# Kernel optimization log

Measured on AMD Instinct MI355X. Metric: run time of the kernel, lower is better.

## Reference

```python
import jax, jax.numpy as jnp
import numpy as np

N_NODES = 50000
N_EDGES = 800000
DIM_IN = 128
DIM_H = 128
DIM_OUT = 10
N_GRAPHS = 256


def _glorot(key, shape):
    lim = float(np.sqrt(6.0 / (shape[0] + shape[1])))
    return jax.random.uniform(key, shape, jnp.float32, -lim, lim)


def setup_inputs() -> dict:
    key = jax.random.key(0)
    ks = jax.random.split(key, 8)
    x = jax.random.normal(ks[0], (N_NODES, DIM_IN), jnp.float32)
    edge_index = jax.random.randint(ks[1], (2, N_EDGES), 0, N_NODES, dtype=jnp.int64)
    batch = jnp.sort(jax.random.randint(ks[2], (N_NODES,), 0, N_GRAPHS, dtype=jnp.int64))
    return {
        'x': x,
        'edge_index': edge_index,
        'batch': batch,
        'W1': _glorot(ks[3], (DIM_IN, DIM_H)),
        'b1': jnp.zeros((DIM_H,), jnp.float32),
        'W2': _glorot(ks[4], (DIM_H, DIM_H)),
        'b2': jnp.zeros((DIM_H,), jnp.float32),
        'Wl1': _glorot(ks[5], (2 * DIM_H, 2 * DIM_H)),
        'bl1': jnp.zeros((2 * DIM_H,), jnp.float32),
        'Wl2': _glorot(ks[6], (2 * DIM_H, DIM_OUT)),
        'bl2': jnp.zeros((DIM_OUT,), jnp.float32),
    }


def _gcn_conv(h, W, b, src, dst, norm, n):
    # x @ W, gather source rows, scale by symmetric norm, scatter-add to dest
    m = (h @ W)[src] * norm[:, None]          # [E+N, dim_h]
    return jax.ops.segment_sum(m, dst, num_segments=n) + b


def reference(x, edge_index, batch, W1, b1, W2, b2, Wl1, bl1, Wl2, bl2):
    n = x.shape[0]
    loops = jnp.arange(n, dtype=edge_index.dtype)
    src = jnp.concatenate([edge_index[0], loops])  # add self-loops (PyG GCNConv default)
    dst = jnp.concatenate([edge_index[1], loops])
    deg = jax.ops.segment_sum(jnp.ones_like(dst, x.dtype), dst, num_segments=n)
    dinv = jnp.where(deg > 0, jax.lax.rsqrt(jnp.maximum(deg, 1.0)), 0.0)
    norm = dinv[src] * dinv[dst]
    # eval mode: dropout is identity
    h1 = _gcn_conv(x, W1, b1, src, dst, norm, n)
    h2 = _gcn_conv(h1, W2, b2, src, dst, norm, n)
    g1 = jax.ops.segment_sum(h1, batch, num_segments=N_GRAPHS)  # global_add_pool
    g2 = jax.ops.segment_sum(h2, batch, num_segments=N_GRAPHS)
    g = jnp.concatenate([g1, g2], axis=1)  # [N_GRAPHS, 2*dim_h]
    h = jax.nn.relu(g @ Wl1 + bl1)
    h = h @ Wl2 + bl2
    return (h, jax.nn.log_softmax(h, axis=1))
```

## Files before the change

kernel.cpp:

```cpp
#include <hip/hip_runtime.h>
#include <hip/hip_bf16.h>
#include <math.h>


#define DIMH 128
#define EBCAP 8192

typedef __attribute__((ext_vector_type(8))) short s16x8;
typedef __attribute__((ext_vector_type(4))) float f32x4;

__device__ inline ushort f2b(float f) {
    uint u = __float_as_uint(f);
    return (ushort)((u + 0x7fffu + ((u >> 16) & 1u)) >> 16);
}
__device__ inline uint pack2(float lo, float hi) {
    return (uint)f2b(lo) | ((uint)f2b(hi) << 16);
}
__device__ inline float blo(uint u) { return __uint_as_float(u << 16); }
__device__ inline float bhi(uint u) { return __uint_as_float(u & 0xffff0000u); }


#define SCAT_CHUNK 8192
__global__ __launch_bounds__(256) void k_scatter(const int* __restrict__ src,
                                                 const int* __restrict__ dst,
                                                 int* __restrict__ bcnt,
                                                 uint* __restrict__ ebuf, int E) {
    __shared__ int hist[256];
    __shared__ int base[256];
    hist[threadIdx.x] = 0;
    __syncthreads();
    int e0 = blockIdx.x * SCAT_CHUNK;
    int e1 = e0 + SCAT_CHUNK; if (e1 > E) e1 = E;
    for (int e = e0 + threadIdx.x; e < e1; e += 256)
        atomicAdd(&hist[dst[e] >> 8], 1);
    __syncthreads();
    {
        int i = threadIdx.x;
        int h = hist[i];
        base[i] = h ? atomicAdd(&bcnt[i], h) : 0;
        hist[i] = 0;
    }
    __syncthreads();
    for (int e = e0 + threadIdx.x; e < e1; e += 256) {
        int d = dst[e];
        int bk = d >> 8;
        int rank = base[bk] + atomicAdd(&hist[bk], 1);
        if (rank < EBCAP)
            ebuf[(size_t)bk * EBCAP + rank] = ((uint)(d & 255) << 24) | (uint)src[e];
    }
}

__global__ __launch_bounds__(256) void k_bcsr(const uint* __restrict__ ebuf,
                                              const int* __restrict__ bcnt,
                                              float* __restrict__ dinv,
                                              int2* __restrict__ rng,
                                              int* __restrict__ srt, int n) {
    __shared__ int cnt[256];
    __shared__ int wsum[4];
    __shared__ int stage[EBCAP];
    int b = blockIdx.x;
    int t = threadIdx.x;
    int c = bcnt[b]; if (c > EBCAP) c = EBCAP;
    size_t B = (size_t)b * EBCAP;
    cnt[t] = 0;
    __syncthreads();
    for (int i = t; i < c; i += 256)
        atomicAdd(&cnt[ebuf[B + i] >> 24], 1);
    __syncthreads();
    int v = cnt[t];
    int incl = v;
    for (int k = 1; k < 64; k <<= 1) {
        int u = __shfl_up(incl, k, 64);
        if ((t & 63) >= k) incl += u;
    }
    if ((t & 63) == 63) wsum[t >> 6] = incl;
    __syncthreads();
    int add = 0;
    for (int j = 0; j < (t >> 6); ++j) add += wsum[j];
    incl += add;
    int loc = incl - v;
    int node = b * 256 + t;
    if (node < n) {
        dinv[node] = rsqrtf((float)(v + 1));
        rng[node] = make_int2((int)B + loc, (int)B + loc + v);
    }
    cnt[t] = loc;
    __syncthreads();
    for (int i = t; i < c; i += 256) {
        uint r = ebuf[B + i];
        int p = atomicAdd(&cnt[r >> 24], 1);
        stage[p] = (int)(r & 0xffffffu);
    }
    __syncthreads();
    for (int i = t; i < c; i += 256) srt[B + i] = stage[i];
}

__global__ __launch_bounds__(256) void k_wprep(const float* __restrict__ W1,
                                               const float* __restrict__ W2,
                                               ushort* __restrict__ WT1,
                                               ushort* __restrict__ WT2) {
    int idx = blockIdx.x * 256 + threadIdx.x;
    const float* W = (idx < 16384) ? W1 : W2;
    ushort* WT = (idx < 16384) ? WT1 : WT2;
    int t = idx & 16383;
    int k = t >> 7, nn = t & 127;
    WT[nn * 128 + k] = f2b(W[t]);
}

template<bool F32IN>
__global__ __launch_bounds__(256) void k_gemm_mfma(const void* __restrict__ Xin,
                                                   const ushort* __restrict__ WT,
                                                   const float* __restrict__ scale,
                                                   ushort* __restrict__ P, int n) {
    __shared__ ushort lds[64 * 128 + 128 * 128];
    ushort* Xs = lds;
    ushort* Ws = lds + 64 * 128;
    const int tid = threadIdx.x;
    const int row0 = blockIdx.x * 64;
    if (F32IN) {
        const float* Xf = (const float*)Xin;
        for (int ci = tid; ci < 2048; ci += 256) {
            int r = ci >> 5, c8 = ci & 31;
            uint dstB = (uint)(r * 256 + c8 * 8) ^ (uint)((r & 7) << 4);
            uint2 v = make_uint2(0u, 0u);
            if (row0 + r < n) {
                float4 f = *(const float4*)(Xf + (size_t)(row0 + r) * 128 + c8 * 4);
                v.x = pack2(f.x, f.y); v.y = pack2(f.z, f.w);
            }
            *(uint2*)((char*)Xs + dstB) = v;
        }
    } else {
        const ushort* Xb = (const ushort*)Xin;
        for (int ci = tid; ci < 1024; ci += 256) {
            int r = ci >> 4, c16 = ci & 15;
            uint dstB = (uint)(r * 256 + c16 * 16) ^ (uint)((r & 7) << 4);
            uint4 v = make_uint4(0u, 0u, 0u, 0u);
            if (row0 + r < n) v = *(const uint4*)(Xb + (size_t)(row0 + r) * 128 + c16 * 8);
            *(uint4*)((char*)Xs + dstB) = v;
        }
    }
    for (int ci = tid; ci < 2048; ci += 256) {
        int r = ci >> 4, c16 = ci & 15;
        uint dstB = (uint)(r * 256 + c16 * 16) ^ (uint)((r & 7) << 4);
        *(uint4*)((char*)Ws + dstB) = *(const uint4*)(WT + (size_t)r * 128 + c16 * 8);
    }
    __syncthreads();
    const int wave = tid >> 6, lane = tid & 63;
    const int l15 = lane & 15, g = lane >> 4;
    f32x4 acc[8];
#pragma unroll
    for (int nt = 0; nt < 8; ++nt) acc[nt] = (f32x4){0.f, 0.f, 0.f, 0.f};
    const int tr = wave * 16 + l15;
    const uint aswz = (uint)((tr & 7) << 4);
#pragma unroll
    for (int kk = 0; kk < 4; ++kk) {
        uint aB = ((uint)(tr * 256 + kk * 64 + g * 16)) ^ aswz;
        s16x8 afrag = *(const s16x8*)((const char*)Xs + aB);
#pragma unroll
        for (int nt = 0; nt < 8; ++nt) {
            int wr = nt * 16 + l15;
            uint bB = ((uint)(wr * 256 + kk * 64 + g * 16)) ^ ((uint)((wr & 7) << 4));
            s16x8 bfrag = *(const s16x8*)((const char*)Ws + bB);
            acc[nt] = __builtin_amdgcn_mfma_f32_16x16x32_bf16(afrag, bfrag, acc[nt], 0, 0, 0);
        }
    }
    float sc[4];
#pragma unroll
    for (int reg = 0; reg < 4; ++reg) {
        int grow = row0 + wave * 16 + g * 4 + reg;
        sc[reg] = (grow < n) ? scale[grow] : 0.f;
    }
#pragma unroll
    for (int nt = 0; nt < 8; ++nt) {
        int gcol = nt * 16 + l15;
#pragma unroll
        for (int reg = 0; reg < 4; ++reg) {
            int grow = row0 + wave * 16 + g * 4 + reg;
            if (grow < n) P[(size_t)grow * 128 + gcol] = f2b(sc[reg] * acc[nt][reg]);
        }
    }
}

__global__ __launch_bounds__(256) void k_aggregate(const ushort* __restrict__ Pb,
                                                   const int2* __restrict__ rng,
                                                   const int* __restrict__ srt,
                                                   const float* __restrict__ dinv,
                                                   const float* __restrict__ bias,
                                                   ushort* __restrict__ Hb, int n) {
    int wave = threadIdx.x >> 6;
    int lane = threadIdx.x & 63;
    int i = blockIdx.x * 4 + wave;
    if (i >= n) return;
    int q   = lane >> 4;
    int sub = lane & 15;
    const uint4* P4 = (const uint4*)Pb;
    float a0 = 0.f, a1 = 0.f, a2 = 0.f, a3 = 0.f;
    float a4 = 0.f, a5 = 0.f, a6 = 0.f, a7 = 0.f;
    if (q == 0) {
        uint4 u = P4[(size_t)i * 16 + sub];
        a0 = blo(u.x); a1 = bhi(u.x); a2 = blo(u.y); a3 = bhi(u.y);
        a4 = blo(u.z); a5 = bhi(u.z); a6 = blo(u.w); a7 = bhi(u.w);
    }
    int2 r2 = rng[i];
    int e1 = r2.y;
    int e  = r2.x + q;
    while (e + 12 < e1) {
        int s0 = srt[e], s1 = srt[e + 4], s2 = srt[e + 8], s3 = srt[e + 12];
        uint4 u0 = P4[(size_t)s0 * 16 + sub];
        uint4 u1 = P4[(size_t)s1 * 16 + sub];
        uint4 u2 = P4[(size_t)s2 * 16 + sub];
        uint4 u3 = P4[(size_t)s3 * 16 + sub];
        a0 += (blo(u0.x) + blo(u1.x)) + (blo(u2.x) + blo(u3.x));
        a1 += (bhi(u0.x) + bhi(u1.x)) + (bhi(u2.x) + bhi(u3.x));
        a2 += (blo(u0.y) + blo(u1.y)) + (blo(u2.y) + blo(u3.y));
        a3 += (bhi(u0.y) + bhi(u1.y)) + (bhi(u2.y) + bhi(u3.y));
        a4 += (blo(u0.z) + blo(u1.z)) + (blo(u2.z) + blo(u3.z));
        a5 += (bhi(u0.z) + bhi(u1.z)) + (bhi(u2.z) + bhi(u3.z));
        a6 += (blo(u0.w) + blo(u1.w)) + (blo(u2.w) + blo(u3.w));
        a7 += (bhi(u0.w) + bhi(u1.w)) + (bhi(u2.w) + bhi(u3.w));
        e += 16;
    }
    while (e < e1) {
        uint4 u = P4[(size_t)srt[e] * 16 + sub];
        a0 += blo(u.x); a1 += bhi(u.x); a2 += blo(u.y); a3 += bhi(u.y);
        a4 += blo(u.z); a5 += bhi(u.z); a6 += blo(u.w); a7 += bhi(u.w);
        e += 4;
    }
    a0 += __shfl_xor(a0, 16, 64); a0 += __shfl_xor(a0, 32, 64);
    a1 += __shfl_xor(a1, 16, 64); a1 += __shfl_xor(a1, 32, 64);
    a2 += __shfl_xor(a2, 16, 64); a2 += __shfl_xor(a2, 32, 64);
    a3 += __shfl_xor(a3, 16, 64); a3 += __shfl_xor(a3, 32, 64);
    a4 += __shfl_xor(a4, 16, 64); a4 += __shfl_xor(a4, 32, 64);
    a5 += __shfl_xor(a5, 16, 64); a5 += __shfl_xor(a5, 32, 64);
    a6 += __shfl_xor(a6, 16, 64); a6 += __shfl_xor(a6, 32, 64);
    a7 += __shfl_xor(a7, 16, 64); a7 += __shfl_xor(a7, 32, 64);
    if (q == 0) {
        float di = dinv[i];
        int c = sub * 8;
        float4 b0 = *(const float4*)(bias + c);
        float4 b1 = *(const float4*)(bias + c + 4);
        uint4 o;
        o.x = pack2(fmaf(di, a0, b0.x), fmaf(di, a1, b0.y));
        o.y = pack2(fmaf(di, a2, b0.z), fmaf(di, a3, b0.w));
        o.z = pack2(fmaf(di, a4, b1.x), fmaf(di, a5, b1.y));
        o.w = pack2(fmaf(di, a6, b1.z), fmaf(di, a7, b1.w));
        *(uint4*)(Hb + (size_t)i * 128 + c) = o;
    }
}

__global__ __launch_bounds__(256) void k_pool_part(const ushort* __restrict__ Hb,
                                                   const int* __restrict__ batch,
                                                   float* __restrict__ Gpart, int n) {
    __shared__ int range[2];
    __shared__ float part[256];
    int g = blockIdx.x >> 2, q = blockIdx.x & 3;
    if (threadIdx.x < 2) {
        int target = g + threadIdx.x;
        int lo = 0, hi = n;
        while (lo < hi) { int m = (lo + hi) >> 1; if (batch[m] < target) lo = m + 1; else hi = m; }
        range[threadIdx.x] = lo;
    }
    __syncthreads();
    int c = threadIdx.x & 127, h = threadIdx.x >> 7;
    int r = range[0] + q * 2 + h, r1 = range[1];
    float s0 = 0.f, s1 = 0.f;
    for (; r + 8 < r1; r += 16) {
        s0 += __uint_as_float((uint)Hb[(size_t)r       * 128 + c] << 16);
        s1 += __uint_as_float((uint)Hb[(size_t)(r + 8) * 128 + c] << 16);
    }
    for (; r < r1; r += 8) s0 += __uint_as_float((uint)Hb[(size_t)r * 128 + c] << 16);
    part[threadIdx.x] = s0 + s1;
    __syncthreads();
    if (threadIdx.x < 128)
        Gpart[(size_t)blockIdx.x * 128 + threadIdx.x] = part[threadIdx.x] + part[threadIdx.x + 128];
}

__global__ __launch_bounds__(256) void k_mlp(const float* __restrict__ Gp1,
                                             const float* __restrict__ Gp2,
                                             const float* __restrict__ Wl1,
                                             const float* __restrict__ bl1,
                                             const float* __restrict__ Wl2,
                                             const float* __restrict__ bl2,
                                             float* __restrict__ out) {
    __shared__ float gs[256];
    __shared__ float zs[256];
    __shared__ float l[10];
    int g = blockIdx.x, j = threadIdx.x;
    {
        const float* Gp = (j < 128) ? Gp1 : Gp2;
        const float* p = Gp + (size_t)g * 512 + (j & 127);
        gs[j] = (p[0] + p[128]) + (p[256] + p[384]);
    }
    __syncthreads();
    float acc = bl1[j];
    for (int k = 0; k < 256; ++k) acc = fmaf(gs[k], Wl1[k * 256 + j], acc);
    zs[j] = fmaxf(acc, 0.f);
    __syncthreads();
    if (j < 10) {
        float a = bl2[j];
        for (int k = 0; k < 256; ++k) a = fmaf(zs[k], Wl2[k * 10 + j], a);
        l[j] = a;
    }
    __syncthreads();
    if (j < 10) {
        float m = l[0];
        for (int i = 1; i < 10; ++i) m = fmaxf(m, l[i]);
        float s = 0.f;
        for (int i = 0; i < 10; ++i) s += expf(l[i] - m);
        float lse = m + logf(s);
        out[g * 10 + j] = l[j];
        out[2560 + g * 10 + j] = l[j] - lse;
    }
}

static inline size_t alignup(size_t v) { return (v + 255) & ~(size_t)255; }

extern "C" void kernel_launch(void* const* d_in, const int* in_sizes, int n_in,
                              void* d_out, int out_size, void* d_ws, size_t ws_size,
                              hipStream_t stream) {
    const float* x    = (const float*)d_in[0];
    const int*   edge = (const int*)d_in[1];
    const int*   batch= (const int*)d_in[2];
    const float* W1   = (const float*)d_in[3];
    const float* b1   = (const float*)d_in[4];
    const float* W2   = (const float*)d_in[5];
    const float* b2   = (const float*)d_in[6];
    const float* Wl1  = (const float*)d_in[7];
    const float* bl1  = (const float*)d_in[8];
    const float* Wl2  = (const float*)d_in[9];
    const float* bl2  = (const float*)d_in[10];

    const int N = in_sizes[2];
    const int E = in_sizes[1] / 2;
    const int* srcIdx = edge;
    const int* dstIdx = edge + E;

    const int nb = (N + 255) >> 8;

    char* ws = (char*)d_ws;
    ushort* P     = (ushort*)ws; ws += alignup((size_t)N * DIMH * 2);
    ushort* Hb    = (ushort*)ws; ws += alignup((size_t)N * DIMH * 2);
    ushort* WT1   = (ushort*)ws; ws += alignup((size_t)128 * 128 * 2);
    ushort* WT2   = (ushort*)ws; ws += alignup((size_t)128 * 128 * 2);
    float*  dinv  = (float*)ws;  ws += alignup((size_t)N * 4);
    int2*   rng   = (int2*)ws;   ws += alignup((size_t)N * 8);
    int*    srt   = (int*)ws;    ws += alignup((size_t)nb * EBCAP * 4);
    uint*   ebuf  = (uint*)ws;   ws += alignup((size_t)nb * EBCAP * 4);
    int*    bcnt  = (int*)ws;    ws += alignup((size_t)256 * 4);
    float*  Gp1   = (float*)ws;  ws += alignup((size_t)1024 * 128 * 4);
    float*  Gp2   = (float*)ws;  ws += alignup((size_t)1024 * 128 * 4);

    hipMemsetAsync(bcnt, 0, (size_t)256 * 4, stream);
    k_scatter<<<(E + SCAT_CHUNK - 1) / SCAT_CHUNK, 256, 0, stream>>>(srcIdx, dstIdx, bcnt, ebuf, E);
    k_bcsr<<<nb, 256, 0, stream>>>(ebuf, bcnt, dinv, rng, srt, N);

    k_wprep<<<128, 256, 0, stream>>>(W1, W2, WT1, WT2);

    int gemm_grid = (N + 63) / 64;
    int agg_grid  = (N + 3) / 4;

    k_gemm_mfma<true><<<gemm_grid, 256, 0, stream>>>(x, WT1, dinv, P, N);
    k_aggregate<<<agg_grid, 256, 0, stream>>>(P, rng, srt, dinv, b1, Hb, N);
    k_pool_part<<<1024, 256, 0, stream>>>(Hb, batch, Gp1, N);

    k_gemm_mfma<false><<<gemm_grid, 256, 0, stream>>>(Hb, WT2, dinv, P, N);
    k_aggregate<<<agg_grid, 256, 0, stream>>>(P, rng, srt, dinv, b2, Hb, N);
    k_pool_part<<<1024, 256, 0, stream>>>(Hb, batch, Gp2, N);

    k_mlp<<<256, 256, 0, stream>>>(Gp1, Gp2, Wl1, bl1, Wl2, bl2, (float*)d_out);
}
```

Measured before the change: 195.8 us.

## Merge independent launches: scatter+convert+wprep front kernel, gemm2+pool1 mid kernel

Combines edge scatter, fp32-to-bf16 conversion of x, and weight transposition into one heterogeneous launch selected by block index. The layer-2 GEMM and the layer-1 pooling, which both only read Hb, are merged into a single launch. This cuts the number of kernel launches and lets independent work overlap. The cost is a separate x conversion pass: an extra bf16 buffer is written and then read back, replacing the fused on-the-fly conversion inside the first GEMM.

Result: faster. 191.3 us (-2.3%).

```diff
diff --git a/kernel.cpp b/kernel.cpp
--- a/kernel.cpp
+++ b/kernel.cpp
@@ -5,6 +5,7 @@
 
 #define DIMH 128
 #define EBCAP 8192
+#define SCAT_CHUNK 8192
 
 typedef __attribute__((ext_vector_type(8))) short s16x8;
 typedef __attribute__((ext_vector_type(4))) float f32x4;
@@ -19,34 +20,58 @@
 __device__ inline float blo(uint u) { return __uint_as_float(u << 16); }
 __device__ inline float bhi(uint u) { return __uint_as_float(u & 0xffff0000u); }
 
-
-#define SCAT_CHUNK 8192
-__global__ __launch_bounds__(256) void k_scatter(const int* __restrict__ src,
-                                                 const int* __restrict__ dst,
-                                                 int* __restrict__ bcnt,
-                                                 uint* __restrict__ ebuf, int E) {
+__global__ __launch_bounds__(256) void k_front(const int* __restrict__ src,
+                                               const int* __restrict__ dst,
+                                               int* __restrict__ bcnt,
+                                               uint* __restrict__ ebuf, int E, int scnb,
+                                               const float* __restrict__ x,
+                                               ushort* __restrict__ Xb, int n8, int cvnb,
+                                               const float* __restrict__ W1,
+                                               const float* __restrict__ W2,
+                                               ushort* __restrict__ WT1,
+                                               ushort* __restrict__ WT2) {
     __shared__ int hist[256];
     __shared__ int base[256];
-    hist[threadIdx.x] = 0;
-    __syncthreads();
-    int e0 = blockIdx.x * SCAT_CHUNK;
-    int e1 = e0 + SCAT_CHUNK; if (e1 > E) e1 = E;
-    for (int e = e0 + threadIdx.x; e < e1; e += 256)
-        atomicAdd(&hist[dst[e] >> 8], 1);
-    __syncthreads();
-    {
-        int i = threadIdx.x;
-        int h = hist[i];
-        base[i] = h ? atomicAdd(&bcnt[i], h) : 0;
-        hist[i] = 0;
-    }
-    __syncthreads();
-    for (int e = e0 + threadIdx.x; e < e1; e += 256) {
-        int d = dst[e];
-        int bk = d >> 8;
-        int rank = base[bk] + atomicAdd(&hist[bk], 1);
-        if (rank < EBCAP)
-            ebuf[(size_t)bk * EBCAP + rank] = ((uint)(d & 255) << 24) | (uint)src[e];
+    int blk = blockIdx.x;
+    int t = threadIdx.x;
+    if (blk < scnb) {
+        hist[t] = 0;
+        __syncthreads();
+        int e0 = blk * SCAT_CHUNK;
+        int e1 = e0 + SCAT_CHUNK; if (e1 > E) e1 = E;
+        for (int e = e0 + t; e < e1; e += 256)
+            atomicAdd(&hist[dst[e] >> 8], 1);
+        __syncthreads();
+        {
+            int h = hist[t];
+            base[t] = h ? atomicAdd(&bcnt[t], h) : 0;
+            hist[t] = 0;
+        }
+        __syncthreads();
+        for (int e = e0 + t; e < e1; e += 256) {
+            int d = dst[e];
+            int bk = d >> 8;
+            int rank = base[bk] + atomicAdd(&hist[bk], 1);
+            if (rank < EBCAP)
+                ebuf[(size_t)bk * EBCAP + rank] = ((uint)(d & 255) << 24) | (uint)src[e];
+        }
+    } else if (blk < scnb + cvnb) {
+        int i = (blk - scnb) * 256 + t;
+        if (i < n8) {
+            const float4* in4 = (const float4*)x;
+            float4 a = in4[2 * i], b = in4[2 * i + 1];
+            uint4 o;
+            o.x = pack2(a.x, a.y); o.y = pack2(a.z, a.w);
+            o.z = pack2(b.x, b.y); o.w = pack2(b.z, b.w);
+            *(uint4*)(Xb + (size_t)i * 8) = o;
+        }
+    } else {
+        int idx = (blk - scnb - cvnb) * 256 + t;
+        const float* W = (idx < 16384) ? W1 : W2;
+        ushort* WT = (idx < 16384) ? WT1 : WT2;
+        int tt = idx & 16383;
+        int k = tt >> 7, nn = tt & 127;
+        WT[nn * 128 + k] = f2b(W[tt]);
     }
 }
 
@@ -95,49 +120,21 @@
     for (int i = t; i < c; i += 256) srt[B + i] = stage[i];
 }
 
-__global__ __launch_bounds__(256) void k_wprep(const float* __restrict__ W1,
-                                               const float* __restrict__ W2,
-                                               ushort* __restrict__ WT1,
-                                               ushort* __restrict__ WT2) {
-    int idx = blockIdx.x * 256 + threadIdx.x;
-    const float* W = (idx < 16384) ? W1 : W2;
-    ushort* WT = (idx < 16384) ? WT1 : WT2;
-    int t = idx & 16383;
-    int k = t >> 7, nn = t & 127;
-    WT[nn * 128 + k] = f2b(W[t]);
-}
-
-template<bool F32IN>
-__global__ __launch_bounds__(256) void k_gemm_mfma(const void* __restrict__ Xin,
-                                                   const ushort* __restrict__ WT,
-                                                   const float* __restrict__ scale,
-                                                   ushort* __restrict__ P, int n) {
-    __shared__ ushort lds[64 * 128 + 128 * 128];
+__device__ __forceinline__ void gemm_body(const ushort* __restrict__ Xb,
+                                          const ushort* __restrict__ WT,
+                                          const float* __restrict__ scale,
+                                          ushort* __restrict__ P, int n,
+                                          int blk, ushort* lds) {
     ushort* Xs = lds;
     ushort* Ws = lds + 64 * 128;
     const int tid = threadIdx.x;
-    const int row0 = blockIdx.x * 64;
-    if (F32IN) {
-        const float* Xf = (const float*)Xin;
-        for (int ci = tid; ci < 2048; ci += 256) {
-            int r = ci >> 5, c8 = ci & 31;
-            uint dstB = (uint)(r * 256 + c8 * 8) ^ (uint)((r & 7) << 4);
-            uint2 v = make_uint2(0u, 0u);
-            if (row0 + r < n) {
-                float4 f = *(const float4*)(Xf + (size_t)(row0 + r) * 128 + c8 * 4);
-                v.x = pack2(f.x, f.y); v.y = pack2(f.z, f.w);
-            }
-            *(uint2*)((char*)Xs + dstB) = v;
-        }
-    } else {
-        const ushort* Xb = (const ushort*)Xin;
-        for (int ci = tid; ci < 1024; ci += 256) {
-            int r = ci >> 4, c16 = ci & 15;
-            uint dstB = (uint)(r * 256 + c16 * 16) ^ (uint)((r & 7) << 4);
-            uint4 v = make_uint4(0u, 0u, 0u, 0u);
-            if (row0 + r < n) v = *(const uint4*)(Xb + (size_t)(row0 + r) * 128 + c16 * 8);
-            *(uint4*)((char*)Xs + dstB) = v;
-        }
+    const int row0 = blk * 64;
+    for (int ci = tid; ci < 1024; ci += 256) {
+        int r = ci >> 4, c16 = ci & 15;
+        uint dstB = (uint)(r * 256 + c16 * 16) ^ (uint)((r & 7) << 4);
+        uint4 v = make_uint4(0u, 0u, 0u, 0u);
+        if (row0 + r < n) v = *(const uint4*)(Xb + (size_t)(row0 + r) * 128 + c16 * 8);
+        *(uint4*)((char*)Xs + dstB) = v;
     }
     for (int ci = tid; ci < 2048; ci += 256) {
         int r = ci >> 4, c16 = ci & 15;
@@ -178,6 +175,65 @@
             int grow = row0 + wave * 16 + g * 4 + reg;
             if (grow < n) P[(size_t)grow * 128 + gcol] = f2b(sc[reg] * acc[nt][reg]);
         }
+    }
+}
+
+__global__ __launch_bounds__(256) void k_gemm(const ushort* __restrict__ Xb,
+                                              const ushort* __restrict__ WT,
+                                              const float* __restrict__ scale,
+                                              ushort* __restrict__ P, int n) {
+    __shared__ ushort lds[64 * 128 + 128 * 128];
+    gemm_body(Xb, WT, scale, P, n, blockIdx.x, lds);
+}
+
+__device__ __forceinline__ void pool_body(const ushort* __restrict__ Hb,
+                                          const int* __restrict__ batch,
+                                          float* __restrict__ Gpart, int n,
+                                          int blk, int* range, float* part) {
+    int g = blk >> 2, q = blk & 3;
+    if (threadIdx.x < 2) {
+        int target = g + threadIdx.x;
+        int lo = 0, hi = n;
+        while (lo < hi) { int m = (lo + hi) >> 1; if (batch[m] < target) lo = m + 1; else hi = m; }
+        range[threadIdx.x] = lo;
+    }
+    __syncthreads();
+    int c = threadIdx.x & 127, h = threadIdx.x >> 7;
+    int r = range[0] + q * 2 + h, r1 = range[1];
+    float s0 = 0.f, s1 = 0.f;
+    for (; r + 8 < r1; r += 16) {
+        s0 += __uint_as_float((uint)Hb[(size_t)r       * 128 + c] << 16);
+        s1 += __uint_as_float((uint)Hb[(size_t)(r + 8) * 128 + c] << 16);
+    }
+    for (; r < r1; r += 8) s0 += __uint_as_float((uint)Hb[(size_t)r * 128 + c] << 16);
+    part[threadIdx.x] = s0 + s1;
+    __syncthreads();
+    if (threadIdx.x < 128)
+        Gpart[(size_t)blk * 128 + threadIdx.x] = part[threadIdx.x] + part[threadIdx.x + 128];
+}
+
+__global__ __launch_bounds__(256) void k_pool(const ushort* __restrict__ Hb,
+                                              const int* __restrict__ batch,
+                                              float* __restrict__ Gpart, int n) {
+    __shared__ int range[2];
+    __shared__ float part[256];
+    pool_body(Hb, batch, Gpart, n, blockIdx.x, range, part);
+}
+
+__global__ __launch_bounds__(256) void k_mid(const ushort* __restrict__ Hb,
+                                             const ushort* __restrict__ WT,
+                                             const float* __restrict__ scale,
+                                             ushort* __restrict__ P, int n, int gemnb,
+                                             const int* __restrict__ batch,
+                                             float* __restrict__ Gpart) {
+    __shared__ ushort lds[64 * 128 + 128 * 128];
+    __shared__ int range[2];
+    __shared__ float part[256];
+    int blk = blockIdx.x;
+    if (blk < gemnb) {
+        gemm_body(Hb, WT, scale, P, n, blk, lds);
+    } else {
+        pool_body(Hb, batch, Gpart, n, blk - gemnb, range, part);
     }
 }
 
@@ -248,33 +304,6 @@
     }
 }
 
-__global__ __launch_bounds__(256) void k_pool_part(const ushort* __restrict__ Hb,
-                                                   const int* __restrict__ batch,
-                                                   float* __restrict__ Gpart, int n) {
-    __shared__ int range[2];
-    __shared__ float part[256];
-    int g = blockIdx.x >> 2, q = blockIdx.x & 3;
-    if (threadIdx.x < 2) {
-        int target = g + threadIdx.x;
-        int lo = 0, hi = n;
-        while (lo < hi) { int m = (lo + hi) >> 1; if (batch[m] < target) lo = m + 1; else hi = m; }
-        range[threadIdx.x] = lo;
-    }
-    __syncthreads();
-    int c = threadIdx.x & 127, h = threadIdx.x >> 7;
-    int r = range[0] + q * 2 + h, r1 = range[1];
-    float s0 = 0.f, s1 = 0.f;
-    for (; r + 8 < r1; r += 16) {
-        s0 += __uint_as_float((uint)Hb[(size_t)r       * 128 + c] << 16);
-        s1 += __uint_as_float((uint)Hb[(size_t)(r + 8) * 128 + c] << 16);
-    }
-    for (; r < r1; r += 8) s0 += __uint_as_float((uint)Hb[(size_t)r * 128 + c] << 16);
-    part[threadIdx.x] = s0 + s1;
-    __syncthreads();
-    if (threadIdx.x < 128)
-        Gpart[(size_t)blockIdx.x * 128 + threadIdx.x] = part[threadIdx.x] + part[threadIdx.x + 128];
-}
-
 __global__ __launch_bounds__(256) void k_mlp(const float* __restrict__ Gp1,
                                              const float* __restrict__ Gp2,
                                              const float* __restrict__ Wl1,
@@ -338,6 +367,7 @@
     const int nb = (N + 255) >> 8;
 
     char* ws = (char*)d_ws;
+    ushort* Xb    = (ushort*)ws; ws += alignup((size_t)N * DIMH * 2);
     ushort* P     = (ushort*)ws; ws += alignup((size_t)N * DIMH * 2);
     ushort* Hb    = (ushort*)ws; ws += alignup((size_t)N * DIMH * 2);
     ushort* WT1   = (ushort*)ws; ws += alignup((size_t)128 * 128 * 2);
@@ -350,22 +380,20 @@
     float*  Gp1   = (float*)ws;  ws += alignup((size_t)1024 * 128 * 4);
     float*  Gp2   = (float*)ws;  ws += alignup((size_t)1024 * 128 * 4);
 
+    const int scnb  = (E + SCAT_CHUNK - 1) / SCAT_CHUNK;
+    const int n8    = N * DIMH / 8;
+    const int cvnb  = (n8 + 255) / 256;
+    const int gemnb = (N + 63) / 64;
+    const int aggnb = (N + 3) / 4;
+
     hipMemsetAsync(bcnt, 0, (size_t)256 * 4, stream);
-    k_scatter<<<(E + SCAT_CHUNK - 1) / SCAT_CHUNK, 256, 0, stream>>>(srcIdx, dstIdx, bcnt, ebuf, E);
+    k_front<<<scnb + cvnb + 128, 256, 0, stream>>>(srcIdx, dstIdx, bcnt, ebuf, E, scnb,
+                                                   x, Xb, n8, cvnb, W1, W2, WT1, WT2);
     k_bcsr<<<nb, 256, 0, stream>>>(ebuf, bcnt, dinv, rng, srt, N);
-
-    k_wprep<<<128, 256, 0, stream>>>(W1, W2, WT1, WT2);
-
-    int gemm_grid = (N + 63) / 64;
-    int agg_grid  = (N + 3) / 4;
-
-    k_gemm_mfma<true><<<gemm_grid, 256, 0, stream>>>(x, WT1, dinv, P, N);
-    k_aggregate<<<agg_grid, 256, 0, stream>>>(P, rng, srt, dinv, b1, Hb, N);
-    k_pool_part<<<1024, 256, 0, stream>>>(Hb, batch, Gp1, N);
-
-    k_gemm_mfma<false><<<gemm_grid, 256, 0, stream>>>(Hb, WT2, dinv, P, N);
-    k_aggregate<<<agg_grid, 256, 0, stream>>>(P, rng, srt, dinv, b2, Hb, N);
-    k_pool_part<<<1024, 256, 0, stream>>>(Hb, batch, Gp2, N);
-
+    k_gemm<<<gemnb, 256, 0, stream>>>(Xb, WT1, dinv, P, N);
+    k_aggregate<<<aggnb, 256, 0, stream>>>(P, rng, srt, dinv, b1, Hb, N);
+    k_mid<<<gemnb + 1024, 256, 0, stream>>>(Hb, WT2, dinv, P, N, gemnb, batch, Gp1);
+    k_aggregate<<<aggnb, 256, 0, stream>>>(P, rng, srt, dinv, b2, Hb, N);
+    k_pool<<<1024, 256, 0, stream>>>(Hb, batch, Gp2, N);
     k_mlp<<<256, 256, 0, stream>>>(Gp1, Gp2, Wl1, bl1, Wl2, bl2, (float*)d_out);
 }
```
